# Kernel optimization log

Hardware: AMD Instinct MI355X
Metric: run time of the kernel (lower is better)

## Reference

```python
import jax, jax.numpy as jnp
import numpy as np

THETA = 10000.0
D_K = 128
MAX_SEQ_LEN = 4096
BATCH, HEADS, SEQ = 4, 16, 4096


def _create_rotation_matrix(theta, d_k, max_seq_len):
    # Block-diagonal 2x2 rotation matrices, one per position: (max_seq_len, d_k, d_k)
    k = jnp.arange(d_k // 2)
    inv_freq = theta ** (-2.0 * k / d_k)                      # (d_k/2,)
    m = jnp.arange(max_seq_len, dtype=jnp.float32)
    angles = m[:, None] * inv_freq[None, :]                   # (S, d_k/2)
    c, s = jnp.cos(angles), jnp.sin(angles)
    i = 2 * k
    R = jnp.zeros((max_seq_len, d_k, d_k), dtype=jnp.float32)
    R = R.at[:, i, i].set(c)
    R = R.at[:, i, i + 1].set(-s)
    R = R.at[:, i + 1, i].set(s)
    R = R.at[:, i + 1, i + 1].set(c)
    return R


def setup_inputs() -> dict:
    key = jax.random.key(0)
    k1, = jax.random.split(key, 1)
    X = jax.random.normal(k1, (BATCH, HEADS, SEQ, D_K), dtype=jnp.float32)
    token_positions = jnp.arange(SEQ, dtype=jnp.int64 if jax.config.jax_enable_x64 else jnp.int32)
    rotation_matrix = _create_rotation_matrix(THETA, D_K, MAX_SEQ_LEN)
    return {"X": X, "token_positions": token_positions, "rotation_matrix": rotation_matrix}


def reference(X, token_positions, rotation_matrix):
    # Gather per-position d_k x d_k rotation matrices, then apply as a matmul:
    # out[..., s, j] = sum_i R[pos[s], j, i] * X[..., s, i]
    R = rotation_matrix[token_positions]                      # (seq, d_k, d_k)
    return jnp.einsum('sji,bhsi->bhsj', R, X)
```

## Files before the change

kernel.cpp:

```cpp
#include <hip/hip_runtime.h>
#include <stdint.h>

__global__ void build_cs_table(const float* __restrict__ R,
                               const int* __restrict__ pos,
                               float* __restrict__ tab, int seq) {
    int idx = blockIdx.x * blockDim.x + threadIdx.x;
    int s = idx >> 6;
    int k = idx & 63;
    if (s >= seq) return;
    long p = (long)pos[s];
    const float* rp = R + p * 16384;
    float c  = rp[258 * k];
    float sn = rp[258 * k + 128];
    tab[s * 128 + 2 * k]     = c;
    tab[s * 128 + 2 * k + 1] = sn;
}

__global__ void rope_apply(const float* __restrict__ X,
                           const float* __restrict__ tab,
                           float* __restrict__ out,
                           int seq, long n4) {
    long i = (long)blockIdx.x * blockDim.x + threadIdx.x;
    if (i >= n4) return;
    long e   = i << 2;
    int  d0  = (int)(e & 127);
    long row = e >> 7;
    int  s   = (int)(row % seq);

    float4 x  = *(const float4*)(X + e);
    float4 cs = *(const float4*)(tab + (long)s * 128 + d0);
    float4 o;
    o.x = cs.x * x.x - cs.y * x.y;
    o.y = cs.y * x.x + cs.x * x.y;
    o.z = cs.z * x.z - cs.w * x.w;
    o.w = cs.w * x.z + cs.z * x.w;
    *(float4*)(out + e) = o;
}

__global__ void rope_direct(const float* __restrict__ X,
                            const float* __restrict__ R,
                            const int* __restrict__ pos,
                            float* __restrict__ out,
                            int seq, long n4) {
    long i = (long)blockIdx.x * blockDim.x + threadIdx.x;
    if (i >= n4) return;
    long e   = i << 2;
    int  d0  = (int)(e & 127);
    long row = e >> 7;
    int  s   = (int)(row % seq);
    long p   = (long)pos[s];
    const float* rp = R + p * 16384;

    int k0 = d0 >> 1;
    float c0 = rp[258 * k0];
    float s0 = rp[258 * k0 + 128];
    float c1 = rp[258 * (k0 + 1)];
    float s1 = rp[258 * (k0 + 1) + 128];

    float4 x = *(const float4*)(X + e);
    float4 o;
    o.x = c0 * x.x - s0 * x.y;
    o.y = s0 * x.x + c0 * x.y;
    o.z = c1 * x.z - s1 * x.w;
    o.w = s1 * x.z + c1 * x.w;
    *(float4*)(out + e) = o;
}

extern "C" void kernel_launch(void* const* d_in, const int* in_sizes, int n_in,
                              void* d_out, int out_size, void* d_ws, size_t ws_size,
                              hipStream_t stream) {
    const float* X   = (const float*)d_in[0];
    const int*   pos = (const int*)d_in[1];
    const float* R   = (const float*)d_in[2];
    float* out       = (float*)d_out;

    const long n   = (long)in_sizes[0];
    const int  seq = in_sizes[1];
    const long n4  = n >> 2;

    const size_t tab_bytes = (size_t)seq * 128 * sizeof(float);

    const int blk = 256;
    if (ws_size >= tab_bytes) {
        float* tab = (float*)d_ws;
        int t1 = seq * 64;
        build_cs_table<<<(t1 + blk - 1) / blk, blk, 0, stream>>>(R, pos, tab, seq);
        rope_apply<<<(int)((n4 + blk - 1) / blk), blk, 0, stream>>>(X, tab, out, seq, n4);
    } else {
        rope_direct<<<(int)((n4 + blk - 1) / blk), blk, 0, stream>>>(X, R, pos, out, seq, n4);
    }
}
```

Before: 423.8 us.

## Fuse cos/sin table build into RoPE kernel with one block per position

Replaces the two-kernel table build plus apply with one kernel where each block handles one sequence position, loads that position's cos/sin into shared memory, then loops over all batch*head rows. This removes the workspace table write/read and a kernel launch, and reuses the coefficients from registers. In exchange, only seq (4096) blocks are launched, and each block's loads are strided 512 B chunks spread across rows, which may reduce memory-access efficiency compared with the fully contiguous flat indexing.

```diff
diff --git a/kernel.cpp b/kernel.cpp
--- a/kernel.cpp
+++ b/kernel.cpp
@@ -1,69 +1,47 @@
 #include <hip/hip_runtime.h>
 #include <stdint.h>
 
-__global__ void build_cs_table(const float* __restrict__ R,
-                               const int* __restrict__ pos,
-                               float* __restrict__ tab, int seq) {
-    int idx = blockIdx.x * blockDim.x + threadIdx.x;
-    int s = idx >> 6;
-    int k = idx & 63;
-    if (s >= seq) return;
-    long p = (long)pos[s];
+__global__ __launch_bounds__(256) void rope_fused(
+        const float* __restrict__ X,
+        const float* __restrict__ R,
+        const int* __restrict__ pos,
+        float* __restrict__ out,
+        int seq, int bh) {
+    __shared__ float cs[128];
+
+    const int s = blockIdx.x;
+    const int t = threadIdx.x;
+
+    const long p = (long)pos[s];
     const float* rp = R + p * 16384;
-    float c  = rp[258 * k];
-    float sn = rp[258 * k + 128];
-    tab[s * 128 + 2 * k]     = c;
-    tab[s * 128 + 2 * k + 1] = sn;
-}
+    if (t < 64) {
+        cs[2 * t] = rp[258 * t];
+    } else if (t < 128) {
+        int k = t - 64;
+        cs[2 * k + 1] = rp[258 * k + 128];
+    }
+    __syncthreads();
 
-__global__ void rope_apply(const float* __restrict__ X,
-                           const float* __restrict__ tab,
-                           float* __restrict__ out,
-                           int seq, long n4) {
-    long i = (long)blockIdx.x * blockDim.x + threadIdx.x;
-    if (i >= n4) return;
-    long e   = i << 2;
-    int  d0  = (int)(e & 127);
-    long row = e >> 7;
-    int  s   = (int)(row % seq);
+    const int d4 = t & 31;
+    const float4 c4 = *(const float4*)(cs + (d4 << 2));
 
-    float4 x  = *(const float4*)(X + e);
-    float4 cs = *(const float4*)(tab + (long)s * 128 + d0);
-    float4 o;
-    o.x = cs.x * x.x - cs.y * x.y;
-    o.y = cs.y * x.x + cs.x * x.y;
-    o.z = cs.z * x.z - cs.w * x.w;
-    o.w = cs.w * x.z + cs.z * x.w;
-    *(float4*)(out + e) = o;
-}
+    const long rstride = (long)seq * 128;
+    const float* Xs = X + (long)s * 128 + (d4 << 2);
+    float*       Os = out + (long)s * 128 + (d4 << 2);
 
-__global__ void rope_direct(const float* __restrict__ X,
-                            const float* __restrict__ R,
-                            const int* __restrict__ pos,
-                            float* __restrict__ out,
-                            int seq, long n4) {
-    long i = (long)blockIdx.x * blockDim.x + threadIdx.x;
-    if (i >= n4) return;
-    long e   = i << 2;
-    int  d0  = (int)(e & 127);
-    long row = e >> 7;
-    int  s   = (int)(row % seq);
-    long p   = (long)pos[s];
-    const float* rp = R + p * 16384;
-
-    int k0 = d0 >> 1;
-    float c0 = rp[258 * k0];
-    float s0 = rp[258 * k0 + 128];
-    float c1 = rp[258 * (k0 + 1)];
-    float s1 = rp[258 * (k0 + 1) + 128];
-
-    float4 x = *(const float4*)(X + e);
-    float4 o;
-    o.x = c0 * x.x - s0 * x.y;
-    o.y = s0 * x.x + c0 * x.y;
-    o.z = c1 * x.z - s1 * x.w;
-    o.w = s1 * x.z + c1 * x.w;
-    *(float4*)(out + e) = o;
+    const int nvec = bh * 32;
+#pragma unroll 4
+    for (int idx = t; idx < nvec; idx += 256) {
+        const int row = idx >> 5;
+        const long e = (long)row * rstride;
+        float4 x = *(const float4*)(Xs + e);
+        float4 o;
+        o.x = c4.x * x.x - c4.y * x.y;
+        o.y = c4.y * x.x + c4.x * x.y;
+        o.z = c4.z * x.z - c4.w * x.w;
+        o.w = c4.w * x.z + c4.z * x.w;
+        *(float4*)(Os + e) = o;
+    }
 }
 
 extern "C" void kernel_launch(void* const* d_in, const int* in_sizes, int n_in,
@@ -76,17 +54,7 @@
 
     const long n   = (long)in_sizes[0];
     const int  seq = in_sizes[1];
-    const long n4  = n >> 2;
+    const int  bh  = (int)(n / ((long)seq * 128));
 
-    const size_t tab_bytes = (size_t)seq * 128 * sizeof(float);
-
-    const int blk = 256;
-    if (ws_size >= tab_bytes) {
-        float* tab = (float*)d_ws;
-        int t1 = seq * 64;
-        build_cs_table<<<(t1 + blk - 1) / blk, blk, 0, stream>>>(R, pos, tab, seq);
-        rope_apply<<<(int)((n4 + blk - 1) / blk), blk, 0, stream>>>(X, tab, out, seq, n4);
-    } else {
-        rope_direct<<<(int)((n4 + blk - 1) / blk), blk, 0, stream>>>(X, R, pos, out, seq, n4);
-    }
+    rope_fused<<<seq, 256, 0, stream>>>(X, R, pos, out, seq, bh);
 }
```

New measurement: 433.2 us. +2.2%, slower.
